# Kernel optimization log

Hardware: AMD Instinct MI355X
Metric: run time of the kernel (lower is better)

## Reference

```python
import jax, jax.numpy as jnp
import numpy as np


def setup_inputs() -> dict:
    key = jax.random.key(0)
    k1, k2, k3, k4, k5 = jax.random.split(key, 5)
    B, C, T, N = 32, 1024, 1024, 3
    video = jax.random.normal(k1, (B, C, T, 1, 1), dtype=jnp.float32)
    length = jax.random.randint(k2, (B,), 1, T + 1).astype(jnp.int32)
    center = 0.5 * jax.random.normal(k3, (N,), dtype=jnp.float32)
    delta = 0.01 * jax.random.normal(k4, (N,), dtype=jnp.float32)
    gamma = 0.0001 * jax.random.normal(k5, (N,), dtype=jnp.float32)
    return {"video": video, "length": length, "center": center,
            "delta": delta, "gamma": gamma}


def reference(video, length, center, delta, gamma):
    B, C, T = video.shape[0], video.shape[1], video.shape[2]
    N = center.shape[0]
    v = video.reshape(B, C, T)
    c = jnp.tanh(center)                                  # (N,)
    g = jnp.tanh(gamma)                                   # (N,)
    lf = length.astype(jnp.float32)                       # (B,)
    # per-(batch, filter) Cauchy center; delta is multiplied by zeros in the
    # original code and therefore has no effect on the output.
    centers = (lf[:, None] - 1.0) * (c[None, :] + 1.0) / 2.0   # (B, N)
    gammas = jnp.exp(1.5 - 2.0 * jnp.abs(g))              # (N,)
    t = jnp.arange(T, dtype=jnp.float32)                  # (T,)
    diff = (t[None, None, :] - centers[:, :, None]) / gammas[None, :, None]
    f = 1.0 / (jnp.pi * gammas[None, :, None] * (1.0 + diff * diff))  # (B,N,T)
    f = f / (jnp.sum(f, axis=2, keepdims=True) + 1e-6)
    # pooled output: for each batch/channel, N weighted time-averages
    o = jnp.einsum('bnt,bct->bcn', f, v)                  # (B, C, N)
    return o.reshape(B, C * N)
```

## Files before the change

### kernel.cpp

```cpp
#include <hip/hip_runtime.h>
#include <math.h>

constexpr int B = 32;
constexpr int C = 1024;
constexpr int T = 1024;
constexpr int N = 3;
constexpr int CPB = 16;
constexpr int CPW = 4;

__device__ __forceinline__ float wred(float x) {
#pragma unroll
  for (int off = 32; off > 0; off >>= 1) x += __shfl_down(x, off);
  return x;
}

__device__ __forceinline__ float dot4(const float4 a, const float4 b) {
  return a.x * b.x + a.y * b.y + a.z * b.z + a.w * b.w;
}

__global__ __launch_bounds__(256) void tsf_fused(
    const float* __restrict__ v ,
    const int* __restrict__ length,
    const float* __restrict__ center,
    const float* __restrict__ gamma_,
    float* __restrict__ out ) {
  const int groups_per_b = C / CPB;
  const int b = blockIdx.x / groups_per_b;
  const int cg = blockIdx.x % groups_per_b;
  const int lane = threadIdx.x & 63;
  const int wv = threadIdx.x >> 6;
  const int ch0 = cg * CPB + wv * CPW;

  const float4* row0 = (const float4*)(v + ((size_t)b * C + ch0 + 0) * T);
  const float4* row1 = (const float4*)(v + ((size_t)b * C + ch0 + 1) * T);
  const float4* row2 = (const float4*)(v + ((size_t)b * C + ch0 + 2) * T);
  const float4* row3 = (const float4*)(v + ((size_t)b * C + ch0 + 3) * T);

  float4 xa0 = row0[lane];
  float4 xa1 = row0[lane + 64];
  float4 xa2 = row0[lane + 128];
  float4 xa3 = row0[lane + 192];
  float4 xb0 = row1[lane];
  float4 xb1 = row1[lane + 64];
  float4 xb2 = row1[lane + 128];
  float4 xb3 = row1[lane + 192];

  const float lf = (float)length[b];
  float4 w[N][4];
  float s[N];
  float pref[N];
#pragma unroll
  for (int n = 0; n < N; ++n) {
    const float c = tanhf(center[n]);
    const float g = tanhf(gamma_[n]);
    const float ctr = (lf - 1.0f) * (c + 1.0f) * 0.5f;
    const float gam = expf(1.5f - 2.0f * fabsf(g));
    const float a = 1.0f / gam;
    const float bb = -ctr * a;
    pref[n] = 1.0f / (3.14159265358979f * gam);
    s[n] = 0.0f;
#pragma unroll
    for (int k = 0; k < 4; ++k) {
      const float t0 = (float)(4 * lane + 256 * k);
      float4 wk;
      float d;
      d = fmaf(t0 + 0.0f, a, bb); wk.x = 1.0f / fmaf(d, d, 1.0f);
      d = fmaf(t0 + 1.0f, a, bb); wk.y = 1.0f / fmaf(d, d, 1.0f);
      d = fmaf(t0 + 2.0f, a, bb); wk.z = 1.0f / fmaf(d, d, 1.0f);
      d = fmaf(t0 + 3.0f, a, bb); wk.w = 1.0f / fmaf(d, d, 1.0f);
      w[n][k] = wk;
      s[n] += (wk.x + wk.y) + (wk.z + wk.w);
    }
  }

  float acc[CPW][N];

#pragma unroll
  for (int n = 0; n < N; ++n)
    acc[0][n] = dot4(xa0, w[n][0]) + dot4(xa1, w[n][1]) +
                dot4(xa2, w[n][2]) + dot4(xa3, w[n][3]);
  xa0 = row2[lane];
  xa1 = row2[lane + 64];
  xa2 = row2[lane + 128];
  xa3 = row2[lane + 192];

#pragma unroll
  for (int n = 0; n < N; ++n)
    acc[1][n] = dot4(xb0, w[n][0]) + dot4(xb1, w[n][1]) +
                dot4(xb2, w[n][2]) + dot4(xb3, w[n][3]);
  xb0 = row3[lane];
  xb1 = row3[lane + 64];
  xb2 = row3[lane + 128];
  xb3 = row3[lane + 192];

#pragma unroll
  for (int n = 0; n < N; ++n)
    acc[2][n] = dot4(xa0, w[n][0]) + dot4(xa1, w[n][1]) +
                dot4(xa2, w[n][2]) + dot4(xa3, w[n][3]);
#pragma unroll
  for (int n = 0; n < N; ++n)
    acc[3][n] = dot4(xb0, w[n][0]) + dot4(xb1, w[n][1]) +
                dot4(xb2, w[n][2]) + dot4(xb3, w[n][3]);

#pragma unroll
  for (int cc = 0; cc < CPW; ++cc)
#pragma unroll
    for (int n = 0; n < N; ++n) acc[cc][n] = wred(acc[cc][n]);
#pragma unroll
  for (int n = 0; n < N; ++n) s[n] = wred(s[n]);

  if (lane == 0) {
#pragma unroll
    for (int n = 0; n < N; ++n) {
      const float scale = pref[n] / fmaf(pref[n], s[n], 1e-6f);
#pragma unroll
      for (int cc = 0; cc < CPW; ++cc)
        out[((size_t)b * C + ch0 + cc) * N + n] = acc[cc][n] * scale;
    }
  }
}

extern "C" void kernel_launch(void* const* d_in, const int* in_sizes, int n_in,
                              void* d_out, int out_size, void* d_ws,
                              size_t ws_size, hipStream_t stream) {
  const float* video = (const float*)d_in[0];
  const int* length = (const int*)d_in[1];
  const float* center = (const float*)d_in[2];
  const float* gamma_ = (const float*)d_in[4];
  float* out = (float*)d_out;

  tsf_fused<<<B * (C / CPB), 256, 0, stream>>>(video, length, center, gamma_,
                                               out);
}
```

Baseline: 30.98 us.

## Stream video rows via async global-to-LDS loads with double-buffered pipeline

```diff
diff --git a/kernel.cpp b/kernel.cpp
--- a/kernel.cpp
+++ b/kernel.cpp
@@ -5,8 +5,8 @@
 constexpr int C = 1024;
 constexpr int T = 1024;
 constexpr int N = 3;
-constexpr int CPB = 16;
-constexpr int CPW = 4;
+constexpr int CPB = 32;
+constexpr int NSTAGE = CPB / 4;
 
 __device__ __forceinline__ float wred(float x) {
 #pragma unroll
@@ -18,36 +18,50 @@
   return a.x * b.x + a.y * b.y + a.z * b.z + a.w * b.w;
 }
 
-__global__ __launch_bounds__(256) void tsf_fused(
+__device__ __forceinline__ void waitv4() {
+  asm volatile("s_waitcnt vmcnt(4)" ::: "memory");
+}
+__device__ __forceinline__ void waitv0() {
+  asm volatile("s_waitcnt vmcnt(0)" ::: "memory");
+}
+
+__global__ __launch_bounds__(256, 4) void tsf_fused(
     const float* __restrict__ v ,
     const int* __restrict__ length,
     const float* __restrict__ center,
     const float* __restrict__ gamma_,
     float* __restrict__ out ) {
-  const int groups_per_b = C / CPB;
-  const int b = blockIdx.x / groups_per_b;
-  const int cg = blockIdx.x % groups_per_b;
+  const int b = blockIdx.x >> 5;
+  const int cg = blockIdx.x & 31;
   const int lane = threadIdx.x & 63;
   const int wv = threadIdx.x >> 6;
-  const int ch0 = cg * CPB + wv * CPW;
+  const int ch_base = cg * CPB;
 
-  const float4* row0 = (const float4*)(v + ((size_t)b * C + ch0 + 0) * T);
-  const float4* row1 = (const float4*)(v + ((size_t)b * C + ch0 + 1) * T);
-  const float4* row2 = (const float4*)(v + ((size_t)b * C + ch0 + 2) * T);
-  const float4* row3 = (const float4*)(v + ((size_t)b * C + ch0 + 3) * T);
+  __shared__ float buf[2][4][T];
 
-  float4 xa0 = row0[lane];
-  float4 xa1 = row0[lane + 64];
-  float4 xa2 = row0[lane + 128];
-  float4 xa3 = row0[lane + 192];
-  float4 xb0 = row1[lane];
-  float4 xb1 = row1[lane + 64];
-  float4 xb2 = row1[lane + 128];
-  float4 xb3 = row1[lane + 192];
+  const float* vbase = v + (size_t)b * C * T;
+
+  auto stage_issue = [&](int s) {
+    const int ch = ch_base + s * 4 + wv;
+    const float* row = vbase + (size_t)ch * T;
+    float* ldsrow = &buf[s & 1][wv][0];
+#pragma unroll
+    for (int it = 0; it < 4; ++it) {
+      __builtin_amdgcn_global_load_lds(
+          (const __attribute__((address_space(1))) void*)(row +
+                                                          4 * (lane + 64 * it)),
+          (__attribute__((address_space(3))) void*)(ldsrow +
+                                                    4 * (lane + 64 * it)),
+          16, 0, 0);
+    }
+  };
+
+  stage_issue(0);
+  stage_issue(1);
 
   const float lf = (float)length[b];
   float4 w[N][4];
-  float s[N];
+  float s_[N];
   float pref[N];
 #pragma unroll
   for (int n = 0; n < N; ++n) {
@@ -58,7 +72,7 @@
     const float a = 1.0f / gam;
     const float bb = -ctr * a;
     pref[n] = 1.0f / (3.14159265358979f * gam);
-    s[n] = 0.0f;
+    s_[n] = 0.0f;
 #pragma unroll
     for (int k = 0; k < 4; ++k) {
       const float t0 = (float)(4 * lane + 256 * k);
@@ -69,53 +83,43 @@
       d = fmaf(t0 + 2.0f, a, bb); wk.z = 1.0f / fmaf(d, d, 1.0f);
       d = fmaf(t0 + 3.0f, a, bb); wk.w = 1.0f / fmaf(d, d, 1.0f);
       w[n][k] = wk;
-      s[n] += (wk.x + wk.y) + (wk.z + wk.w);
+      s_[n] += (wk.x + wk.y) + (wk.z + wk.w);
     }
   }
 
-  float acc[CPW][N];
+  float acc[NSTAGE][N];
+#pragma unroll
+  for (int s = 0; s < NSTAGE; ++s) {
+    if (s < NSTAGE - 1) waitv4();
+    else waitv0();
+    const float4* src = (const float4*)&buf[s & 1][wv][0];
+    const float4 x0 = src[lane];
+    const float4 x1 = src[lane + 64];
+    const float4 x2 = src[lane + 128];
+    const float4 x3 = src[lane + 192];
+#pragma unroll
+    for (int n = 0; n < N; ++n)
+      acc[s][n] = dot4(x0, w[n][0]) + dot4(x1, w[n][1]) +
+                  dot4(x2, w[n][2]) + dot4(x3, w[n][3]);
+    if (s + 2 < NSTAGE) stage_issue(s + 2);
+  }
 
 #pragma unroll
-  for (int n = 0; n < N; ++n)
-    acc[0][n] = dot4(xa0, w[n][0]) + dot4(xa1, w[n][1]) +
-                dot4(xa2, w[n][2]) + dot4(xa3, w[n][3]);
-  xa0 = row2[lane];
-  xa1 = row2[lane + 64];
-  xa2 = row2[lane + 128];
-  xa3 = row2[lane + 192];
-
+  for (int s = 0; s < NSTAGE; ++s)
 #pragma unroll
-  for (int n = 0; n < N; ++n)
-    acc[1][n] = dot4(xb0, w[n][0]) + dot4(xb1, w[n][1]) +
-                dot4(xb2, w[n][2]) + dot4(xb3, w[n][3]);
-  xb0 = row3[lane];
-  xb1 = row3[lane + 64];
-  xb2 = row3[lane + 128];
-  xb3 = row3[lane + 192];
-
+    for (int n = 0; n < N; ++n) acc[s][n] = wred(acc[s][n]);
 #pragma unroll
-  for (int n = 0; n < N; ++n)
-    acc[2][n] = dot4(xa0, w[n][0]) + dot4(xa1, w[n][1]) +
-                dot4(xa2, w[n][2]) + dot4(xa3, w[n][3]);
-#pragma unroll
-  for (int n = 0; n < N; ++n)
-    acc[3][n] = dot4(xb0, w[n][0]) + dot4(xb1, w[n][1]) +
-                dot4(xb2, w[n][2]) + dot4(xb3, w[n][3]);
-
-#pragma unroll
-  for (int cc = 0; cc < CPW; ++cc)
-#pragma unroll
-    for (int n = 0; n < N; ++n) acc[cc][n] = wred(acc[cc][n]);
-#pragma unroll
-  for (int n = 0; n < N; ++n) s[n] = wred(s[n]);
+  for (int n = 0; n < N; ++n) s_[n] = wred(s_[n]);
 
   if (lane == 0) {
 #pragma unroll
     for (int n = 0; n < N; ++n) {
-      const float scale = pref[n] / fmaf(pref[n], s[n], 1e-6f);
+      const float scale = pref[n] / fmaf(pref[n], s_[n], 1e-6f);
 #pragma unroll
-      for (int cc = 0; cc < CPW; ++cc)
-        out[((size_t)b * C + ch0 + cc) * N + n] = acc[cc][n] * scale;
+      for (int s = 0; s < NSTAGE; ++s) {
+        const int ch = ch_base + s * 4 + wv;
+        out[((size_t)b * C + ch) * N + n] = acc[s][n] * scale;
+      }
     }
   }
 }
```

Measured after the change: 60.21 us. +94.3%, slower.
